# Kernel tuning notes

Hardware: AMD Instinct MI355X
Metric: run time of the kernel (lower is better)

## Reference

```python
import jax, jax.numpy as jnp
import numpy as np

B, S, D, H, E, K = 4, 512, 1024, 16, 4, 2
HD = D // H
LN_EPS = 1e-5


def setup_inputs() -> dict:
    key = jax.random.key(0)
    ks = jax.random.split(key, 16)
    def w(k, shape, fan_in):
        return jax.random.normal(k, shape, jnp.float32) / np.float32(np.sqrt(fan_in))
    return {
        "x": jax.random.normal(ks[0], (B, S, D), jnp.float32),
        # stacked per-expert attention params [E, D, D] / [E, D]
        "Wq": w(ks[1], (E, D, D), D), "bq": jnp.zeros((E, D), jnp.float32),
        "Wk": w(ks[2], (E, D, D), D), "bk": jnp.zeros((E, D), jnp.float32),
        "Wv": w(ks[3], (E, D, D), D), "bv": jnp.zeros((E, D), jnp.float32),
        "Wo": w(ks[4], (E, D, D), D), "bo": jnp.zeros((E, D), jnp.float32),
        # router: Linear(D->D/2), LayerNorm, relu, Linear(D/2->E)
        "Wr1": w(ks[5], (D, D // 2), D), "br1": jnp.zeros((D // 2,), jnp.float32),
        "ln_g": jnp.ones((D // 2,), jnp.float32), "ln_b": jnp.zeros((D // 2,), jnp.float32),
        "Wr2": w(ks[6], (D // 2, E), D // 2), "br2": jnp.zeros((E,), jnp.float32),
    }


def _moe_attention(x, Wq, bq, Wk, bk, Wv, bv, Wo, bo, Wr1, br1, ln_g, ln_b, Wr2, br2):
    # ---- router ----
    h = x @ Wr1 + br1                                        # [B,S,D/2]
    mu = jnp.mean(h, axis=-1, keepdims=True)
    var = jnp.var(h, axis=-1, keepdims=True)
    h = (h - mu) * jax.lax.rsqrt(var + LN_EPS) * ln_g + ln_b
    h = jax.nn.relu(h)
    logits = h @ Wr2 + br2                                   # [B,S,E]
    probs = jax.nn.softmax(logits, axis=-1)
    top_p, top_i = jax.lax.top_k(probs, K)                   # [B,S,K]
    # scatter-add of top-k probs into dense expert mask [B,S,E]
    emask = jnp.sum(jax.nn.one_hot(top_i, E, dtype=x.dtype) * top_p[..., None], axis=2)

    # ---- dense per-expert attention (naive: every expert on every token) ----
    def heads(t):  # [E,B,S,D] -> [E,B,H,S,HD]
        return t.reshape(E, B, S, H, HD).transpose(0, 1, 3, 2, 4)

    q = heads(jnp.einsum('bsd,edf->ebsf', x, Wq) + bq[:, None, None, :])
    k = heads(jnp.einsum('bsd,edf->ebsf', x, Wk) + bk[:, None, None, :])
    v = heads(jnp.einsum('bsd,edf->ebsf', x, Wv) + bv[:, None, None, :])

    scores = jnp.einsum('ebhqd,ebhkd->ebhqk', q, k) / np.float32(np.sqrt(HD))
    attn = jax.nn.softmax(scores, axis=-1)                   # [E,B,H,S,S]
    o = jnp.einsum('ebhqk,ebhkd->ebhqd', attn, v)
    o = o.transpose(0, 1, 3, 2, 4).reshape(E, B, S, D)
    o = jnp.einsum('ebsd,edf->ebsf', o, Wo) + bo[:, None, None, :]  # [E,B,S,D]

    # ---- masked combine ----
    return jnp.einsum('ebsd,bse->bsd', o, emask)


def reference(x, Wq, bq, Wk, bk, Wv, bv, Wo, bo, Wr1, br1, ln_g, ln_b, Wr2, br2):
    return _moe_attention(x, Wq, bq, Wk, bk, Wv, bv, Wo, bo,
                          Wr1, br1, ln_g, ln_b, Wr2, br2)
```

## Files before the change

kernel.cpp:

```cpp
#include <hip/hip_runtime.h>
#include <hip/hip_bf16.h>
#include <math.h>

#define B_   4
#define S_   512
#define D_   1024
#define H_   16
#define E_   4
#define HD_  64
#define D2_  512
#define NTOK (B_*S_)

#define TDE ((size_t)NTOK * D_)
#define WWE ((size_t)D_ * D_)
#define ND2 ((size_t)NTOK * D2_)

typedef unsigned short ushort;
typedef short shortv8 __attribute__((ext_vector_type(8)));
typedef ushort ushortv4 __attribute__((ext_vector_type(4)));
typedef _Float16 halfv8 __attribute__((ext_vector_type(8)));
typedef _Float16 halfv4 __attribute__((ext_vector_type(4)));
typedef float floatv4 __attribute__((ext_vector_type(4)));

__device__ __forceinline__ ushort f2bf(float f) {
    union { __hip_bfloat16 b; ushort u; } cv;
    cv.b = __float2bfloat16(f);
    return cv.u;
}
__device__ __forceinline__ float bf2f(ushort u) {
    union { ushort u; __hip_bfloat16 b; } cv;
    cv.u = u;
    return __bfloat162float(cv.b);
}
__device__ __forceinline__ void gload16(const void* g, void* l) {
    __builtin_amdgcn_global_load_lds(
        (const __attribute__((address_space(1))) unsigned int*)g,
        (__attribute__((address_space(3))) unsigned int*)l, 16, 0, 0);
}

__device__ __forceinline__ void gemm_core_bf_sb(
    const ushort* __restrict__ A0, const ushort* __restrict__ A1,
    const ushort* __restrict__ B0, const ushort* __restrict__ B1,
    int K, int klen, int brow, int bcol, ushort* lds, floatv4 acc[4][4])
{
    const int tid  = threadIdx.x;
    const int wave = tid >> 6, lane = tid & 63;
    const int wm = wave >> 1, wn = wave & 1;
    const int lr = lane & 15, lc = lane >> 4;

    const ushort* gsrc[4] = {A0, A1, B0, B1};
    size_t goff[4][2];
    int    loff[4][2];
#pragma unroll
    for (int t = 0; t < 4; t++) {
#pragma unroll
        for (int s = 0; s < 2; s++) {
            int p = s * 256 + tid;
            int m = p >> 2;
            int c = (p & 3) ^ ((m >> 1) & 3);
            int r = (t < 2) ? (brow + m) : (bcol + m);
            goff[t][s] = (size_t)r * K + c * 8;
            loff[t][s] = t * 4096 + p * 8;
        }
    }

    int aoff[4], boff[4];
#pragma unroll
    for (int i = 0; i < 4; i++) {
        int ra = wm * 64 + i * 16 + lr;
        aoff[i] = ra * 32 + ((lc ^ ((ra >> 1) & 3)) * 8);
        int rb2 = wn * 64 + i * 16 + lr;
        boff[i] = rb2 * 32 + ((lc ^ ((rb2 >> 1) & 3)) * 8);
    }

    for (int k0 = 0; k0 < klen; k0 += 32) {
#pragma unroll
        for (int t = 0; t < 4; t++)
#pragma unroll
            for (int s = 0; s < 2; s++)
                gload16(gsrc[t] + goff[t][s] + k0, lds + loff[t][s]);
        asm volatile("s_waitcnt vmcnt(0)" ::: "memory");
        __builtin_amdgcn_s_barrier();
        __builtin_amdgcn_sched_barrier(0);

        shortv8 ah[4], al[4], bh[4], bl[4];
#pragma unroll
        for (int i = 0; i < 4; i++) {
            ah[i] = *(const shortv8*)(lds +         aoff[i]);
            al[i] = *(const shortv8*)(lds +  4096 + aoff[i]);
            bh[i] = *(const shortv8*)(lds +  8192 + boff[i]);
            bl[i] = *(const shortv8*)(lds + 12288 + boff[i]);
        }
#pragma unroll
        for (int mi = 0; mi < 4; mi++)
#pragma unroll
            for (int nj = 0; nj < 4; nj++) {
                acc[mi][nj] = __builtin_amdgcn_mfma_f32_16x16x32_bf16(ah[mi], bh[nj], acc[mi][nj], 0, 0, 0);
                acc[mi][nj] = __builtin_amdgcn_mfma_f32_16x16x32_bf16(ah[mi], bl[nj], acc[mi][nj], 0, 0, 0);
                acc[mi][nj] = __builtin_amdgcn_mfma_f32_16x16x32_bf16(al[mi], bh[nj], acc[mi][nj], 0, 0, 0);
            }

        asm volatile("s_waitcnt lgkmcnt(0)" ::: "memory");
        __builtin_amdgcn_sched_barrier(0);
        __builtin_amdgcn_s_barrier();
    }
}

__device__ __forceinline__ void gemm_core_h2(
    const _Float16* __restrict__ A0, const _Float16* __restrict__ B0,
    int K, int klen, int brow, int bcol, _Float16* lds, floatv4 acc[8][4])
{
    const int tid  = threadIdx.x;
    const int wave = tid >> 6, lane = tid & 63;
    const int wm = wave >> 1, wn = wave & 1;
    const int lr = lane & 15, lc = lane >> 4;

    size_t goffA[4];
    int    loffA[4];
#pragma unroll
    for (int s = 0; s < 4; s++) {
        int p = s * 256 + tid;
        int m = p >> 2;
        int c = (p & 3) ^ ((m >> 1) & 3);
        goffA[s] = (size_t)(brow + m) * K + c * 8;
        loffA[s] = p * 8;
    }
    size_t goffB[2];
    int    loffB[2];
#pragma unroll
    for (int s = 0; s < 2; s++) {
        int p = s * 256 + tid;
        int m = p >> 2;
        int c = (p & 3) ^ ((m >> 1) & 3);
        goffB[s] = (size_t)(bcol + m) * K + c * 8;
        loffB[s] = 8192 + p * 8;
    }

    int aoff[8], boff[4];
#pragma unroll
    for (int i = 0; i < 8; i++) {
        int ra = wm * 128 + i * 16 + lr;
        aoff[i] = ra * 32 + ((lc ^ ((ra >> 1) & 3)) * 8);
    }
#pragma unroll
    for (int j = 0; j < 4; j++) {
        int rb = wn * 64 + j * 16 + lr;
        boff[j] = 8192 + rb * 32 + ((lc ^ ((rb >> 1) & 3)) * 8);
    }

#define STAGEH_(buf, kk) \
    _Pragma("unroll") for (int s = 0; s < 4; s++) \
        gload16(A0 + goffA[s] + (kk), lds + (buf) * 12288 + loffA[s]); \
    _Pragma("unroll") for (int s = 0; s < 2; s++) \
        gload16(B0 + goffB[s] + (kk), lds + (buf) * 12288 + loffB[s]);

    STAGEH_(0, 0)

    int cur = 0;
    for (int k0 = 0; k0 < klen; k0 += 32, cur ^= 1) {
        if (k0 + 32 < klen) {
            STAGEH_(cur ^ 1, k0 + 32)
            asm volatile("s_waitcnt vmcnt(6)" ::: "memory");
        } else {
            asm volatile("s_waitcnt vmcnt(0)" ::: "memory");
        }
        __builtin_amdgcn_s_barrier();
        __builtin_amdgcn_sched_barrier(0);

        const _Float16* L = lds + cur * 12288;
        halfv8 aa[8], bb[4];
#pragma unroll
        for (int j = 0; j < 4; j++) bb[j] = *(const halfv8*)(L + boff[j]);
#pragma unroll
        for (int i = 0; i < 8; i++) aa[i] = *(const halfv8*)(L + aoff[i]);
#pragma unroll
        for (int mi = 0; mi < 8; mi++)
#pragma unroll
            for (int nj = 0; nj < 4; nj++)
                acc[mi][nj] = __builtin_amdgcn_mfma_f32_16x16x32_f16(aa[mi], bb[nj], acc[mi][nj], 0, 0, 0);

        asm volatile("s_waitcnt lgkmcnt(0)" ::: "memory");
        __builtin_amdgcn_sched_barrier(0);
        __builtin_amdgcn_s_barrier();
    }
#undef STAGEH_
}

#define ACC_INIT4(acc) \
    _Pragma("unroll") for (int i = 0; i < 4; i++) \
    _Pragma("unroll") for (int j = 0; j < 4; j++) \
    _Pragma("unroll") for (int q = 0; q < 4; q++) acc[i][j][q] = 0.f;

#define ACC_INIT8(acc) \
    _Pragma("unroll") for (int i = 0; i < 8; i++) \
    _Pragma("unroll") for (int j = 0; j < 4; j++) \
    _Pragma("unroll") for (int q = 0; q < 4; q++) acc[i][j][q] = 0.f;

#define EPI_VARS \
    const int lane = threadIdx.x & 63, wave = threadIdx.x >> 6; \
    const int wm = wave >> 1, wn = wave & 1, lr = lane & 15, lc = lane >> 4;

__global__ __launch_bounds__(256, 3) void gemm_mega(
    const ushort* __restrict__ xh, const ushort* __restrict__ xl,
    const ushort* __restrict__ wr1h, const ushort* __restrict__ wr1l,
    float* __restrict__ hpart,
    const _Float16* __restrict__ xf, const _Float16* __restrict__ wth,
    const float* __restrict__ bq, const float* __restrict__ bk, const float* __restrict__ bv,
    _Float16* __restrict__ qf, _Float16* __restrict__ kf, _Float16* __restrict__ vf)
{
    __shared__ ushort smem[24576];
    const int bid = blockIdx.x;
    const int xcd = bid & 7, j = bid >> 3;

    if (j < 32) {
        const int u = xcd * 32 + j;
        const int kz = u >> 6;
        const int rem = u & 63;
        const int brow = (rem >> 2) * 128, bcol = (rem & 3) * 128;

        floatv4 acc[4][4];
        ACC_INIT4(acc)
        const int koff = kz * 256;
        gemm_core_bf_sb(xh + koff, xl + koff, wr1h + koff, wr1l + koff,
                        D_, 256, brow, bcol, smem, acc);

        float* C = hpart + (size_t)kz * ND2;
        EPI_VARS
#pragma unroll
        for (int mi = 0; mi < 4; mi++)
#pragma unroll
            for (int nj = 0; nj < 4; nj++)
#pragma unroll
                for (int i = 0; i < 4; i++) {
                    int row = brow + wm * 64 + mi * 16 + lc * 4 + i;
                    int col = bcol + wn * 64 + nj * 16 + lr;
                    C[(size_t)row * D2_ + col] = acc[mi][nj][i];
                }
    } else if (j < 96) {
        const int u = xcd * 64 + (j - 32);
        const int z = u >> 6;
        const int rem = u & 63;
        const int brow = (rem >> 3) * 256, bcol = (rem & 7) * 128;
        const int slot = z >> 1, m = z & 1;
        const size_t so = (size_t)slot * TDE;
        const _Float16* Bm = wth + (size_t)(slot * 4 + 1 + m) * WWE;
        const float* bias = ((m == 0) ? bk : bv) + (size_t)slot * D_;
        _Float16* Oo = ((m == 0) ? kf : vf) + so;

        floatv4 acc[8][4];
        ACC_INIT8(acc)
        gemm_core_h2(xf, Bm, D_, D_, brow, bcol, (_Float16*)smem, acc);

        EPI_VARS
#pragma unroll
        for (int mi = 0; mi < 8; mi++)
#pragma unroll
            for (int nj = 0; nj < 4; nj++)
#pragma unroll
                for (int i = 0; i < 4; i++) {
                    int row = brow + wm * 128 + mi * 16 + lc * 4 + i;
                    int col = bcol + wn * 64 + nj * 16 + lr;
                    Oo[(size_t)row * D_ + col] = (_Float16)(acc[mi][nj][i] + bias[col]);
                }
    } else {
        const int u = xcd * 32 + (j - 96);
        const int e = u >> 6;
        const int rem = u & 63;
        const int brow = (rem >> 3) * 256, bcol = (rem & 7) * 128;
        const _Float16* Bm = wth + (size_t)(e * 4 + 0) * WWE;
        const float* bias = bq + (size_t)e * D_;
        _Float16* Oo = qf + (size_t)e * TDE;

        floatv4 acc[8][4];
        ACC_INIT8(acc)
        gemm_core_h2(xf, Bm, D_, D_, brow, bcol, (_Float16*)smem, acc);

        EPI_VARS
#pragma unroll
        for (int mi = 0; mi < 8; mi++)
#pragma unroll
            for (int nj = 0; nj < 4; nj++)
#pragma unroll
                for (int i = 0; i < 4; i++) {
                    int row = brow + wm * 128 + mi * 16 + lc * 4 + i;
                    int col = bcol + wn * 64 + nj * 16 + lr;
                    Oo[(size_t)row * D_ + col] =
                        (_Float16)((acc[mi][nj][i] + bias[col]) * 0.125f);
                }
    }
}

__global__ __launch_bounds__(256, 3) void gemm_combine4(
    const _Float16* __restrict__ oh,
    const _Float16* __restrict__ wth,
    const float* __restrict__ bo, const float* __restrict__ emask,
    const int* __restrict__ idx, const int* __restrict__ meta,
    float* __restrict__ out2)
{
    __shared__ _Float16 lds[24576];
    const int lid = blockIdx.x + 8 * (blockIdx.y + 8 * blockIdx.z);
    const int nid = (lid & 7) * 32 + (lid >> 3);
    const int e = nid >> 6;
    const int rem = nid & 63;
    const int brow = (rem >> 3) * 256, bcol = (rem & 7) * 128;

    const int pcnt = meta[32 + e];
    if (brow >= pcnt) return;
    const size_t so = (size_t)e * TDE;
    const _Float16* Bm = wth + (size_t)(e * 4 + 3) * WWE;
    const float* bias = bo + (size_t)e * D_;
    const int* idxe = idx + e * 2048;

    floatv4 acc[8][4];
    ACC_INIT8(acc)
    gemm_core_h2(oh + so, Bm, D_, D_, brow, bcol, lds, acc);

    EPI_VARS
#pragma unroll
    for (int mi = 0; mi < 8; mi++)
#pragma unroll
        for (int nj = 0; nj < 4; nj++)
#pragma unroll
            for (int i = 0; i < 4; i++) {
                int srow = brow + wm * 128 + mi * 16 + lc * 4 + i;
                int raw = idxe[srow];
                if (raw >= 0) {
                    int row = raw & 0xFFFF;
                    int rank = (raw >> 30) & 1;
                    float s = emask[(size_t)row * E_ + e];
                    int col = bcol + wn * 64 + nj * 16 + lr;
                    out2[(size_t)rank * TDE + (size_t)row * D_ + col] =
                        s * (acc[mi][nj][i] + bias[col]);
                }
            }
}

__global__ __launch_bounds__(256) void reduce_out(
    const float* __restrict__ out2, float* __restrict__ out)
{
    size_t i = (size_t)blockIdx.x * 256 + threadIdx.x;
    const float4* p = (const float4*)out2;
    float4 a = p[i], b = p[i + TDE / 4];
    float4 r;
    r.x = a.x + b.x;
    r.y = a.y + b.y;
    r.z = a.z + b.z;
    r.w = a.w + b.w;
    ((float4*)out)[i] = r;
}

__global__ __launch_bounds__(256) void build_lists(
    const float* __restrict__ emask, int* __restrict__ idx, int* __restrict__ meta)
{
    const int e = blockIdx.x;
    const int tid = threadIdx.x;
    __shared__ int scan[256];
    __shared__ int runsh;
    if (tid == 0) runsh = 0;
    int* idxe = idx + e * 2048;

    for (int b = 0; b < B_; b++) {
        __syncthreads();
        const int base = runsh;
        int t0 = b * 512 + tid * 2;
        int f0 = (emask[(size_t)t0 * E_ + e] != 0.f) ? 1 : 0;
        int f1 = (emask[(size_t)(t0 + 1) * E_ + e] != 0.f) ? 1 : 0;
        int my = f0 + f1;
        scan[tid] = my;
        __syncthreads();
        for (int off = 1; off < 256; off <<= 1) {
            int v = (tid >= off) ? scan[tid - off] : 0;
            __syncthreads();
            scan[tid] += v;
            __syncthreads();
        }
        int excl = scan[tid] - my;
        int cnt = scan[255];
        if (f0) {
            int rank = 0;
            for (int ep = 0; ep < e; ep++)
                if (emask[(size_t)t0 * E_ + ep] != 0.f) rank = 1;
            idxe[base + excl] = t0 | (rank << 30);
        }
        if (f1) {
            int rank = 0;
            for (int ep = 0; ep < e; ep++)
                if (emask[(size_t)(t0 + 1) * E_ + ep] != 0.f) rank = 1;
            idxe[base + excl + f0] = (t0 + 1) | (rank << 30);
        }
        int plen = (cnt + 63) & ~63;
        for (int i = cnt + tid; i < plen; i += 256)
            idxe[base + i] = (b * 512) | (int)0x80000000;
        if (tid == 0) {
            meta[e * 4 + b] = base;
            meta[16 + e * 4 + b] = plen >> 6;
            runsh = base + plen;
        }
    }
    __syncthreads();
    int total = runsh;
    if (tid == 0) meta[32 + e] = total;
    for (int i = total + tid; i < 2048; i += 256)
        idxe[i] = (int)0x80000000;
}

__global__ __launch_bounds__(256, 3) void attn_all(
    const _Float16* __restrict__ qf_, const _Float16* __restrict__ kf_,
    const _Float16* __restrict__ vf_,
    _Float16* __restrict__ oh_,
    const int* __restrict__ idx, const int* __restrict__ meta)
{
    const int lid = blockIdx.x + 8 * (blockIdx.y + 64 * blockIdx.z);
    const int nid = (lid & 7) * 256 + (lid >> 3);
    const int e = nid >> 9;
    const int rem = nid & 511;
    const int bhid = rem >> 3, qtile = rem & 7;
    const int bb = bhid >> 4, hh = bhid & 15;

    const int ptiles = meta[16 + e * 4 + bb];
    if (qtile >= ptiles) return;
    const int pstart = meta[e * 4 + bb];

    __shared__ _Float16 Kf[128 * 64];
    __shared__ _Float16 Vt[64 * 128];
    __shared__ _Float16 Pw[4][16 * 128];

    const size_t zo = (size_t)e * TDE;
    const int tid = threadIdx.x;
    const int wave = tid >> 6, lane = tid & 63;
    const int lr = lane & 15, lc = lane >> 4;
    const int q0 = pstart + qtile * 64;
    const size_t kvbase = zo + (size_t)bb * S_ * D_ + hh * 64;

    halfv8 qq[2];
    {
        int slot = q0 + wave * 16 + lr;
        int tok = idx[e * 2048 + slot] & 0xFFFF;
        size_t qoff = zo + (size_t)tok * D_ + hh * 64 + lc * 8;
        qq[0] = *(const halfv8*)(qf_ + qoff);
        qq[1] = *(const halfv8*)(qf_ + qoff + 32);
    }

    floatv4 ov[4];
    float m4[4], l4[4];
#pragma unroll
    for (int df = 0; df < 4; df++)
#pragma unroll
        for (int i = 0; i < 4; i++) ov[df][i] = 0.f;
#pragma unroll
    for (int i = 0; i < 4; i++) { m4[i] = -3.0e38f; l4[i] = 0.f; }

    halfv8 vr[2][2];
#define LOADV_(kk0_) \
    _Pragma("unroll") for (int pp = 0; pp < 2; pp++) { \
        const _Float16* vsrc = vf_ + kvbase + (size_t)((kk0_) + pp * 64 + lane) * D_ + wave * 16; \
        vr[pp][0] = *(const halfv8*)vsrc; \
        vr[pp][1] = *(const halfv8*)(vsrc + 8); \
    }

    LOADV_(0)

    for (int kt = 0; kt < S_ / 128; kt++) {
        const int kk0 = kt * 128;
        __syncthreads();

#pragma unroll
        for (int s = 0; s < 4; s++) {
            int p = s * 256 + tid;
            int r = p >> 3;
            int c = (p & 7) ^ (r & 7);
            gload16(kf_ + kvbase + (size_t)(kk0 + r) * D_ + c * 8, Kf + p * 8);
        }
#pragma unroll
        for (int pp = 0; pp < 2; pp++) {
            int k = pp * 64 + lane;
            int kc = k >> 3, kl = k & 7;
#pragma unroll
            for (int h = 0; h < 2; h++)
#pragma unroll
                for (int jj = 0; jj < 8; jj++) {
                    int d = wave * 16 + h * 8 + jj;
                    Vt[d * 128 + ((kc ^ jj) << 3) + kl] = vr[pp][h][jj];
                }
        }
        __syncthreads();

        if (kt + 1 < S_ / 128) { LOADV_(kk0 + 128) }

        floatv4 sc[8];
#pragma unroll
        for (int n = 0; n < 8; n++)
#pragma unroll
            for (int i = 0; i < 4; i++) sc[n][i] = 0.f;
        __builtin_amdgcn_s_setprio(1);
#pragma unroll
        for (int n = 0; n < 8; n++)
#pragma unroll
            for (int ds = 0; ds < 2; ds++) {
                int off = (16 * n + lr) * 64 + (((ds * 4 + lc) ^ (lr & 7)) * 8);
                halfv8 kr = *(const halfv8*)(Kf + off);
                sc[n] = __builtin_amdgcn_mfma_f32_16x16x32_f16(qq[ds], kr, sc[n], 0, 0, 0);
            }
        __builtin_amdgcn_s_setprio(0);

        float tm[4];
#pragma unroll
        for (int i = 0; i < 4; i++) {
            float a = fmaxf(fmaxf(sc[0][i], sc[1][i]), fmaxf(sc[2][i], sc[3][i]));
            float b = fmaxf(fmaxf(sc[4][i], sc[5][i]), fmaxf(sc[6][i], sc[7][i]));
            tm[i] = fmaxf(a, b);
        }
#pragma unroll
        for (int off = 1; off <= 8; off <<= 1)
#pragma unroll
            for (int i = 0; i < 4; i++)
                tm[i] = fmaxf(tm[i], __shfl_xor(tm[i], off));

        float nm[4], sca[4], ps[4];
#pragma unroll
        for (int i = 0; i < 4; i++) {
            nm[i] = fmaxf(m4[i], tm[i]);
            sca[i] = __expf(m4[i] - nm[i]);
            ps[i] = 0.f;
        }
#pragma unroll
        for (int n = 0; n < 8; n++)
#pragma unroll
            for (int i = 0; i < 4; i++) {
                float p = __expf(sc[n][i] - nm[i]);
                ps[i] += p;
                int q = lc * 4 + i;
                int kcol = 16 * n + lr;
                Pw[wave][q * 128 + (((kcol >> 3) ^ (q & 7)) << 3) + (kcol & 7)] =
                    (_Float16)p;
            }
#pragma unroll
        for (int off = 1; off <= 8; off <<= 1)
#pragma unroll
            for (int i = 0; i < 4; i++)
                ps[i] += __shfl_xor(ps[i], off);
#pragma unroll
        for (int i = 0; i < 4; i++) {
            l4[i] = l4[i] * sca[i] + ps[i];
            m4[i] = nm[i];
        }
#pragma unroll
        for (int df = 0; df < 4; df++)
#pragma unroll
            for (int i = 0; i < 4; i++) ov[df][i] *= sca[i];

        asm volatile("s_waitcnt lgkmcnt(0)" ::: "memory");
        __builtin_amdgcn_sched_barrier(0);

        __builtin_amdgcn_s_setprio(1);
#pragma unroll
        for (int ks = 0; ks < 4; ks++) {
            int ch = ((ks * 4 + lc) ^ (lr & 7)) * 8;
            halfv8 pa = *(const halfv8*)(&Pw[wave][lr * 128 + ch]);
#pragma unroll
            for (int df = 0; df < 4; df++) {
                halfv8 vfr = *(const halfv8*)(Vt + (df * 16 + lr) * 128 + ch);
                ov[df] = __builtin_amdgcn_mfma_f32_16x16x32_f16(pa, vfr, ov[df], 0, 0, 0);
            }
        }
        __builtin_amdgcn_s_setprio(0);
    }
#undef LOADV_

    const size_t qobase = zo + hh * 64;
#pragma unroll
    for (int df = 0; df < 4; df++)
#pragma unroll
        for (int i = 0; i < 4; i++) {
            float val = ov[df][i] / l4[i];
            size_t off = qobase + (size_t)(q0 + wave * 16 + lc * 4 + i) * D_ + df * 16 + lr;
            oh_[off] = (_Float16)val;
        }
}

__global__ __launch_bounds__(256) void prep_all(
    const float* __restrict__ x,
    ushort* __restrict__ hb, ushort* __restrict__ lb, _Float16* __restrict__ hf,
    const float* __restrict__ Wr1, ushort* __restrict__ wr1h, ushort* __restrict__ wr1l,
    const float* __restrict__ Wq, const float* __restrict__ Wk,
    const float* __restrict__ Wv, const float* __restrict__ Wo,
    _Float16* __restrict__ Th)
{
    __shared__ float tile[64][65];
    const int bid = blockIdx.x;
    const int tid = threadIdx.x;

    if (bid < 2048) {
        int i = bid * 256 + tid;
        float4 v = ((const float4*)x)[i];
        float vv[4] = {v.x, v.y, v.z, v.w};
        ushortv4 hv, lv;
        halfv4 hhv;
#pragma unroll
        for (int j = 0; j < 4; j++) {
            ushort h = f2bf(vv[j]);
            hv[j] = h;
            lv[j] = f2bf(vv[j] - bf2f(h));
            hhv[j] = (_Float16)vv[j];
        }
        ((ushortv4*)hb)[i] = hv;
        ((ushortv4*)lb)[i] = lv;
        ((halfv4*)hf)[i] = hhv;
    } else if (bid < 2176) {
        int u = bid - 2048;
        int n0 = (u & 7) * 64, k0 = (u >> 3) * 64;
#pragma unroll
        for (int i = 0; i < 16; i++) {
            int p = i * 256 + tid;
            int r = p >> 6, c = p & 63;
            tile[r][c] = Wr1[(size_t)(k0 + r) * D2_ + n0 + c];
        }
        __syncthreads();
#pragma unroll
        for (int i = 0; i < 16; i++) {
            int p = i * 256 + tid;
            int rn = p >> 6, ck = p & 63;
            float v = tile[ck][rn];
            ushort h = f2bf(v);
            wr1h[(size_t)(n0 + rn) * D_ + k0 + ck] = h;
            wr1l[(size_t)(n0 + rn) * D_ + k0 + ck] = f2bf(v - bf2f(h));
        }
    } else {
        int u = bid - 2176;
        int xg = u & 15, yg = (u >> 4) & 15, mg = u >> 8;
        const int e = mg >> 2, m = mg & 3;
        const float* W = ((m == 0) ? Wq : (m == 1) ? Wk : (m == 2) ? Wv : Wo)
                         + (size_t)e * WWE;
        _Float16* T = Th + (size_t)mg * WWE;
        const int n0 = xg * 64, k0 = yg * 64;
#pragma unroll
        for (int i = 0; i < 16; i++) {
            int p = i * 256 + tid;
            int r = p >> 6, c = p & 63;
            tile[r][c] = W[(size_t)(k0 + r) * D_ + n0 + c];
        }
        __syncthreads();
#pragma unroll
        for (int i = 0; i < 16; i++) {
            int p = i * 256 + tid;
            int rn = p >> 6, ck = p & 63;
            T[(size_t)(n0 + rn) * D_ + k0 + ck] = (_Float16)tile[ck][rn];
        }
    }
}

__global__ __launch_bounds__(256) void router_post(
    const float* __restrict__ hpart, const float* __restrict__ br1,
    const float* __restrict__ ln_g, const float* __restrict__ ln_b,
    const float* __restrict__ Wr2, const float* __restrict__ br2,
    float* __restrict__ emask)
{
    const int t = blockIdx.x;
    const int tid = threadIdx.x;
    __shared__ float red[256];
    __shared__ float logits[E_];

    const float* hp = hpart + (size_t)t * D2_;
    float x0 = hp[tid] + hp[ND2 + tid] + hp[2 * ND2 + tid] + hp[3 * ND2 + tid] + br1[tid];
    float x1 = hp[tid + 256] + hp[ND2 + tid + 256] + hp[2 * ND2 + tid + 256]
             + hp[3 * ND2 + tid + 256] + br1[tid + 256];

    red[tid] = x0 + x1; __syncthreads();
    for (int off = 128; off; off >>= 1) { if (tid < off) red[tid] += red[tid + off]; __syncthreads(); }
    float mu = red[0] * (1.f / 512.f);
    __syncthreads();

    float d0 = x0 - mu, d1 = x1 - mu;
    red[tid] = d0 * d0 + d1 * d1; __syncthreads();
    for (int off = 128; off; off >>= 1) { if (tid < off) red[tid] += red[tid + off]; __syncthreads(); }
    float rs = rsqrtf(red[0] * (1.f / 512.f) + 1e-5f);
    __syncthreads();

    float n0 = fmaxf(fmaf(d0 * rs, ln_g[tid],       ln_b[tid]),       0.f);
    float n1 = fmaxf(fmaf(d1 * rs, ln_g[tid + 256], ln_b[tid + 256]), 0.f);

    for (int e = 0; e < E_; e++) {
        red[tid] = n0 * Wr2[(size_t)tid * E_ + e] + n1 * Wr2[(size_t)(tid + 256) * E_ + e];
        __syncthreads();
        for (int off = 128; off; off >>= 1) { if (tid < off) red[tid] += red[tid + off]; __syncthreads(); }
        if (tid == 0) logits[e] = red[0] + br2[e];
        __syncthreads();
    }

    if (tid == 0) {
        float mx = fmaxf(fmaxf(logits[0], logits[1]), fmaxf(logits[2], logits[3]));
        float p[E_], sum = 0.f;
        for (int e = 0; e < E_; e++) { p[e] = expf(logits[e] - mx); sum += p[e]; }
        float inv = 1.f / sum;
        for (int e = 0; e < E_; e++) p[e] *= inv;
        int i1 = 0;
        for (int e = 1; e < E_; e++) if (p[e] > p[i1]) i1 = e;
        int i2 = -1;
        for (int e = 0; e < E_; e++) { if (e == i1) continue; if (i2 < 0 || p[e] > p[i2]) i2 = e; }
        float o[E_] = {0.f, 0.f, 0.f, 0.f};
        o[i1] = p[i1]; o[i2] = p[i2];
        for (int e = 0; e < E_; e++) emask[(size_t)t * E_ + e] = o[e];
    }
}

extern "C" void kernel_launch(void* const* d_in, const int* in_sizes, int n_in,
                              void* d_out, int out_size, void* d_ws, size_t ws_size,
                              hipStream_t stream) {
    const float* x   = (const float*)d_in[0];
    const float* Wq  = (const float*)d_in[1];
    const float* bq  = (const float*)d_in[2];
    const float* Wk  = (const float*)d_in[3];
    const float* bk  = (const float*)d_in[4];
    const float* Wv  = (const float*)d_in[5];
    const float* bv  = (const float*)d_in[6];
    const float* Wo  = (const float*)d_in[7];
    const float* bo  = (const float*)d_in[8];
    const float* Wr1 = (const float*)d_in[9];
    const float* br1 = (const float*)d_in[10];
    const float* lng = (const float*)d_in[11];
    const float* lnb = (const float*)d_in[12];
    const float* Wr2 = (const float*)d_in[13];
    const float* br2 = (const float*)d_in[14];

    float* out = (float*)d_out;
    char* w = (char*)d_ws;
    dim3 blk(256);
    const size_t MB = 1024ull * 1024ull;

    float*    emask = (float*)w;
    int*      idx   = (int*)(w + 64 * 1024);
    int*      meta  = (int*)(w + 96 * 1024);
    _Float16* wth   = (_Float16*)(w + 1 * MB);
    ushort*   wr1h  = (ushort*)(w + 33 * MB);
    ushort*   wr1l  = (ushort*)(w + 34 * MB);
    ushort*   xh    = (ushort*)(w + 35 * MB);
    ushort*   xl    = (ushort*)(w + 39 * MB);
    _Float16* xfh   = (_Float16*)(w + 43 * MB);
    float*    hpart = (float*)(w + 47 * MB);
    _Float16* qfb   = (_Float16*)(w + 63 * MB);
    _Float16* kfb   = (_Float16*)(w + 79 * MB);
    _Float16* vfb   = (_Float16*)(w + 95 * MB);
    _Float16* ohb   = (_Float16*)(w + 111 * MB);
    float*    out2  = (float*)(w + 127 * MB);

    prep_all<<<dim3(6272), blk, 0, stream>>>(
        x, xh, xl, xfh, Wr1, wr1h, wr1l, Wq, Wk, Wv, Wo, wth);

    gemm_mega<<<dim3(1024), blk, 0, stream>>>(
        xh, xl, wr1h, wr1l, hpart, xfh, wth, bq, bk, bv, qfb, kfb, vfb);

    router_post<<<dim3(NTOK), blk, 0, stream>>>(hpart, br1, lng, lnb, Wr2, br2, emask);
    build_lists<<<dim3(E_), blk, 0, stream>>>(emask, idx, meta);

    attn_all<<<dim3(8, 64, 4), blk, 0, stream>>>(
        qfb, kfb, vfb, ohb, idx, meta);

    gemm_combine4<<<dim3(8, 8, 4), blk, 0, stream>>>(
        ohb, wth, bo, emask, idx, meta, out2);
    reduce_out<<<dim3(TDE / 1024), blk, 0, stream>>>(out2, out);
}
```

Baseline: 213.2 us.

## Double attention query tile to 128 rows per block to reuse K/V tiles

Each attention block now handles 128 gathered query rows (two 16-row groups per wave) instead of 64, so every K/V tile staged in shared memory serves twice as many queries and the V fragment loads are shared across both groups. Token lists are padded to multiples of 128 to match, the grid is halved, and the occupancy hint drops from 3 to 2 blocks per CU. This cuts K/V global traffic and per-block staging overhead, at the cost of more padded query rows, fewer blocks, higher register and LDS use per block, and lower occupancy.

```diff
diff --git a/kernel.cpp b/kernel.cpp
--- a/kernel.cpp
+++ b/kernel.cpp
@@ -388,12 +388,12 @@
                 if (emask[(size_t)(t0 + 1) * E_ + ep] != 0.f) rank = 1;
             idxe[base + excl + f0] = (t0 + 1) | (rank << 30);
         }
-        int plen = (cnt + 63) & ~63;
+        int plen = (cnt + 127) & ~127;
         for (int i = cnt + tid; i < plen; i += 256)
             idxe[base + i] = (b * 512) | (int)0x80000000;
         if (tid == 0) {
             meta[e * 4 + b] = base;
-            meta[16 + e * 4 + b] = plen >> 6;
+            meta[16 + e * 4 + b] = plen >> 7;
             runsh = base + plen;
         }
     }
@@ -404,17 +404,17 @@
         idxe[i] = (int)0x80000000;
 }
 
-__global__ __launch_bounds__(256, 3) void attn_all(
+__global__ __launch_bounds__(256, 2) void attn_all(
     const _Float16* __restrict__ qf_, const _Float16* __restrict__ kf_,
     const _Float16* __restrict__ vf_,
     _Float16* __restrict__ oh_,
     const int* __restrict__ idx, const int* __restrict__ meta)
 {
-    const int lid = blockIdx.x + 8 * (blockIdx.y + 64 * blockIdx.z);
-    const int nid = (lid & 7) * 256 + (lid >> 3);
-    const int e = nid >> 9;
-    const int rem = nid & 511;
-    const int bhid = rem >> 3, qtile = rem & 7;
+    const int lid = blockIdx.x + 4 * (blockIdx.y + 64 * blockIdx.z);
+    const int nid = (lid & 7) * 128 + (lid >> 3);
+    const int e = nid >> 8;
+    const int rem = nid & 255;
+    const int bhid = rem >> 2, qtile = rem & 3;
     const int bb = bhid >> 4, hh = bhid & 15;
 
     const int ptiles = meta[16 + e * 4 + bb];
@@ -423,32 +423,37 @@
 
     __shared__ _Float16 Kf[128 * 64];
     __shared__ _Float16 Vt[64 * 128];
-    __shared__ _Float16 Pw[4][16 * 128];
+    __shared__ _Float16 Pw[4][32 * 128];
 
     const size_t zo = (size_t)e * TDE;
     const int tid = threadIdx.x;
     const int wave = tid >> 6, lane = tid & 63;
     const int lr = lane & 15, lc = lane >> 4;
-    const int q0 = pstart + qtile * 64;
+    const int q0 = pstart + qtile * 128;
     const size_t kvbase = zo + (size_t)bb * S_ * D_ + hh * 64;
 
-    halfv8 qq[2];
-    {
-        int slot = q0 + wave * 16 + lr;
+    halfv8 qq[2][2];
+#pragma unroll
+    for (int g = 0; g < 2; g++) {
+        int slot = q0 + wave * 32 + g * 16 + lr;
         int tok = idx[e * 2048 + slot] & 0xFFFF;
         size_t qoff = zo + (size_t)tok * D_ + hh * 64 + lc * 8;
-        qq[0] = *(const halfv8*)(qf_ + qoff);
-        qq[1] = *(const halfv8*)(qf_ + qoff + 32);
-    }
-
-    floatv4 ov[4];
-    float m4[4], l4[4];
-#pragma unroll
-    for (int df = 0; df < 4; df++)
-#pragma unroll
-        for (int i = 0; i < 4; i++) ov[df][i] = 0.f;
-#pragma unroll
-    for (int i = 0; i < 4; i++) { m4[i] = -3.0e38f; l4[i] = 0.f; }
+        qq[g][0] = *(const halfv8*)(qf_ + qoff);
+        qq[g][1] = *(const halfv8*)(qf_ + qoff + 32);
+    }
+
+    floatv4 ov[2][4];
+    float m4[2][4], l4[2][4];
+#pragma unroll
+    for (int g = 0; g < 2; g++)
+#pragma unroll
+        for (int df = 0; df < 4; df++)
+#pragma unroll
+            for (int i = 0; i < 4; i++) ov[g][df][i] = 0.f;
+#pragma unroll
+    for (int g = 0; g < 2; g++)
+#pragma unroll
+        for (int i = 0; i < 4; i++) { m4[g][i] = -3.0e38f; l4[g][i] = 0.f; }
 
     halfv8 vr[2][2];
 #define LOADV_(kk0_) \
@@ -487,67 +492,70 @@
 
         if (kt + 1 < S_ / 128) { LOADV_(kk0 + 128) }
 
-        floatv4 sc[8];
-#pragma unroll
-        for (int n = 0; n < 8; n++)
-#pragma unroll
-            for (int i = 0; i < 4; i++) sc[n][i] = 0.f;
-        __builtin_amdgcn_s_setprio(1);
-#pragma unroll
-        for (int n = 0; n < 8; n++)
-#pragma unroll
-            for (int ds = 0; ds < 2; ds++) {
-                int off = (16 * n + lr) * 64 + (((ds * 4 + lc) ^ (lr & 7)) * 8);
-                halfv8 kr = *(const halfv8*)(Kf + off);
-                sc[n] = __builtin_amdgcn_mfma_f32_16x16x32_f16(qq[ds], kr, sc[n], 0, 0, 0);
+#pragma unroll
+        for (int g = 0; g < 2; g++) {
+            floatv4 sc[8];
+#pragma unroll
+            for (int n = 0; n < 8; n++)
+#pragma unroll
+                for (int i = 0; i < 4; i++) sc[n][i] = 0.f;
+            __builtin_amdgcn_s_setprio(1);
+#pragma unroll
+            for (int n = 0; n < 8; n++)
+#pragma unroll
+                for (int ds = 0; ds < 2; ds++) {
+                    int off = (16 * n + lr) * 64 + (((ds * 4 + lc) ^ (lr & 7)) * 8);
+                    halfv8 kr = *(const halfv8*)(Kf + off);
+                    sc[n] = __builtin_amdgcn_mfma_f32_16x16x32_f16(qq[g][ds], kr, sc[n], 0, 0, 0);
+                }
+            __builtin_amdgcn_s_setprio(0);
+
+            float tm[4];
+#pragma unroll
+            for (int i = 0; i < 4; i++) {
+                float a = fmaxf(fmaxf(sc[0][i], sc[1][i]), fmaxf(sc[2][i], sc[3][i]));
+                float b = fmaxf(fmaxf(sc[4][i], sc[5][i]), fmaxf(sc[6][i], sc[7][i]));
+                tm[i] = fmaxf(a, b);
             }
-        __builtin_amdgcn_s_setprio(0);
-
-        float tm[4];
-#pragma unroll
-        for (int i = 0; i < 4; i++) {
-            float a = fmaxf(fmaxf(sc[0][i], sc[1][i]), fmaxf(sc[2][i], sc[3][i]));
-            float b = fmaxf(fmaxf(sc[4][i], sc[5][i]), fmaxf(sc[6][i], sc[7][i]));
-            tm[i] = fmaxf(a, b);
-        }
-#pragma unroll
-        for (int off = 1; off <= 8; off <<= 1)
-#pragma unroll
-            for (int i = 0; i < 4; i++)
-                tm[i] = fmaxf(tm[i], __shfl_xor(tm[i], off));
-
-        float nm[4], sca[4], ps[4];
-#pragma unroll
-        for (int i = 0; i < 4; i++) {
-            nm[i] = fmaxf(m4[i], tm[i]);
-            sca[i] = __expf(m4[i] - nm[i]);
-            ps[i] = 0.f;
-        }
-#pragma unroll
-        for (int n = 0; n < 8; n++)
+#pragma unroll
+            for (int off = 1; off <= 8; off <<= 1)
+#pragma unroll
+                for (int i = 0; i < 4; i++)
+                    tm[i] = fmaxf(tm[i], __shfl_xor(tm[i], off));
+
+            float nm[4], sca[4], ps[4];
 #pragma unroll
             for (int i = 0; i < 4; i++) {
-                float p = __expf(sc[n][i] - nm[i]);
-                ps[i] += p;
-                int q = lc * 4 + i;
-                int kcol = 16 * n + lr;
-                Pw[wave][q * 128 + (((kcol >> 3) ^ (q & 7)) << 3) + (kcol & 7)] =
-                    (_Float16)p;
+                nm[i] = fmaxf(m4[g][i], tm[i]);
+                sca[i] = __expf(m4[g][i] - nm[i]);
+                ps[i] = 0.f;
             }
 #pragma unroll
-        for (int off = 1; off <= 8; off <<= 1)
-#pragma unroll
-            for (int i = 0; i < 4; i++)
-                ps[i] += __shfl_xor(ps[i], off);
-#pragma unroll
-        for (int i = 0; i < 4; i++) {
-            l4[i] = l4[i] * sca[i] + ps[i];
-            m4[i] = nm[i];
-        }
-#pragma unroll
-        for (int df = 0; df < 4; df++)
-#pragma unroll
-            for (int i = 0; i < 4; i++) ov[df][i] *= sca[i];
+            for (int n = 0; n < 8; n++)
+#pragma unroll
+                for (int i = 0; i < 4; i++) {
+                    float p = __expf(sc[n][i] - nm[i]);
+                    ps[i] += p;
+                    int q = g * 16 + lc * 4 + i;
+                    int kcol = 16 * n + lr;
+                    Pw[wave][q * 128 + (((kcol >> 3) ^ (q & 7)) << 3) + (kcol & 7)] =
+                        (_Float16)p;
+                }
+#pragma unroll
+            for (int off = 1; off <= 8; off <<= 1)
+#pragma unroll
+                for (int i = 0; i < 4; i++)
+                    ps[i] += __shfl_xor(ps[i], off);
+#pragma unroll
+            for (int i = 0; i < 4; i++) {
+                l4[g][i] = l4[g][i] * sca[i] + ps[i];
+                m4[g][i] = nm[i];
+            }
+#pragma unroll
+            for (int df = 0; df < 4; df++)
+#pragma unroll
+                for (int i = 0; i < 4; i++) ov[g][df][i] *= sca[i];
+        }
 
         asm volatile("s_waitcnt lgkmcnt(0)" ::: "memory");
         __builtin_amdgcn_sched_barrier(0);
@@ -556,11 +564,14 @@
 #pragma unroll
         for (int ks = 0; ks < 4; ks++) {
             int ch = ((ks * 4 + lc) ^ (lr & 7)) * 8;
-            halfv8 pa = *(const halfv8*)(&Pw[wave][lr * 128 + ch]);
 #pragma unroll
             for (int df = 0; df < 4; df++) {
                 halfv8 vfr = *(const halfv8*)(Vt + (df * 16 + lr) * 128 + ch);
-                ov[df] = __builtin_amdgcn_mfma_f32_16x16x32_f16(pa, vfr, ov[df], 0, 0, 0);
+#pragma unroll
+                for (int g = 0; g < 2; g++) {
+                    halfv8 pa = *(const halfv8*)(&Pw[wave][(g * 16 + lr) * 128 + ch]);
+                    ov[g][df] = __builtin_amdgcn_mfma_f32_16x16x32_f16(pa, vfr, ov[g][df], 0, 0, 0);
+                }
             }
         }
         __builtin_amdgcn_s_setprio(0);
@@ -569,13 +580,16 @@
 
     const size_t qobase = zo + hh * 64;
 #pragma unroll
-    for (int df = 0; df < 4; df++)
-#pragma unroll
-        for (int i = 0; i < 4; i++) {
-            float val = ov[df][i] / l4[i];
-            size_t off = qobase + (size_t)(q0 + wave * 16 + lc * 4 + i) * D_ + df * 16 + lr;
-            oh_[off] = (_Float16)val;
-        }
+    for (int g = 0; g < 2; g++)
+#pragma unroll
+        for (int df = 0; df < 4; df++)
+#pragma unroll
+            for (int i = 0; i < 4; i++) {
+                float val = ov[g][df][i] / l4[g][i];
+                size_t off = qobase +
+                    (size_t)(q0 + wave * 32 + g * 16 + lc * 4 + i) * D_ + df * 16 + lr;
+                oh_[off] = (_Float16)val;
+            }
 }
 
 __global__ __launch_bounds__(256) void prep_all(
@@ -752,7 +766,7 @@
     router_post<<<dim3(NTOK), blk, 0, stream>>>(hpart, br1, lng, lnb, Wr2, br2, emask);
     build_lists<<<dim3(E_), blk, 0, stream>>>(emask, idx, meta);
 
-    attn_all<<<dim3(8, 64, 4), blk, 0, stream>>>(
+    attn_all<<<dim3(4, 64, 4), blk, 0, stream>>>(
         qfb, kfb, vfb, ohb, idx, meta);
 
     gemm_combine4<<<dim3(8, 8, 4), blk, 0, stream>>>(
```

Result: no change. 209.4 us (-1.8%).
